# Performance work log

Hardware: AMD Instinct MI355X
Metric: run time of the kernel (lower is better)

## Reference

```python
import jax, jax.numpy as jnp
import numpy as np
from jax import lax

NUM_CLASSES = 2
NUM_PROTO = 10
C = 720


def _conv(x, w, b, pad):
    # x: [B,Cin,H,W], w: [Cout,Cin,kh,kw]
    y = lax.conv_general_dilated(x, w, (1, 1), ((pad, pad), (pad, pad)),
                                 dimension_numbers=('NCHW', 'OIHW', 'NCHW'))
    return y + b[None, :, None, None]


def _bn(x, g, b, rm, rv):
    inv = g / jnp.sqrt(rv + 1e-5)
    return (x - rm[None, :, None, None]) * inv[None, :, None, None] + b[None, :, None, None]


def _ln(x, g, b):
    mu = jnp.mean(x, -1, keepdims=True)
    var = jnp.var(x, -1, keepdims=True)
    return (x - mu) / jnp.sqrt(var + 1e-5) * g + b


def _l2n(x):
    n = jnp.linalg.norm(x, axis=-1, keepdims=True)
    return x / jnp.maximum(n, 1e-12)


def _resize_bilinear_ac(x, oh, ow):
    # bilinear with align_corners=True, x: [B,C,H,W]
    B, Cc, H, W = x.shape
    ys = jnp.linspace(0.0, H - 1.0, oh)
    xs = jnp.linspace(0.0, W - 1.0, ow)
    y0 = jnp.floor(ys).astype(jnp.int32)
    y1 = jnp.minimum(y0 + 1, H - 1)
    wy = (ys - y0).astype(x.dtype)
    x0 = jnp.floor(xs).astype(jnp.int32)
    x1 = jnp.minimum(x0 + 1, W - 1)
    wx = (xs - x0).astype(x.dtype)
    r = x[:, :, y0, :] * (1 - wy)[None, None, :, None] + x[:, :, y1, :] * wy[None, None, :, None]
    return r[:, :, :, x0] * (1 - wx) + r[:, :, :, x1] * wx


def setup_inputs() -> dict:
    key = jax.random.key(0)
    ks = jax.random.split(key, 8)
    B, H = 2, 96
    f32 = jnp.float32
    return {
        'feat1': jax.random.normal(ks[0], (B, 48, H, H), f32),
        'feat2': jax.random.normal(ks[1], (B, 96, H // 2, H // 2), f32),
        'feat3': jax.random.normal(ks[2], (B, 192, H // 4, H // 4), f32),
        'feat4': jax.random.normal(ks[3], (B, 384, H // 8, H // 8), f32),
        'cls_w': jax.random.normal(ks[4], (C, C, 3, 3), f32) * 0.02,
        'cls_b': jnp.zeros((C,), f32),
        'cls_bn_g': jnp.ones((C,), f32),
        'cls_bn_b': jnp.zeros((C,), f32),
        'cls_bn_rm': jnp.zeros((C,), f32),
        'cls_bn_rv': jnp.ones((C,), f32),
        'proj_w1': jax.random.normal(ks[5], (C, C, 1, 1), f32) * 0.02,
        'proj_b1': jnp.zeros((C,), f32),
        'proj_bn_g': jnp.ones((C,), f32),
        'proj_bn_b': jnp.zeros((C,), f32),
        'proj_bn_rm': jnp.zeros((C,), f32),
        'proj_bn_rv': jnp.ones((C,), f32),
        'proj_w2': jax.random.normal(ks[6], (C, C, 1, 1), f32) * 0.02,
        'proj_b2': jnp.zeros((C,), f32),
        'ln_feat_g': jnp.ones((C,), f32),
        'ln_feat_b': jnp.zeros((C,), f32),
        'ln_mask_g': jnp.ones((NUM_CLASSES,), f32),
        'ln_mask_b': jnp.zeros((NUM_CLASSES,), f32),
        'prototypes': jax.random.normal(ks[7], (NUM_CLASSES, NUM_PROTO, C), f32) * 0.02,
    }


def reference(feat1, feat2, feat3, feat4, cls_w, cls_b, cls_bn_g, cls_bn_b, cls_bn_rm,
              cls_bn_rv, proj_w1, proj_b1, proj_bn_g, proj_bn_b, proj_bn_rm, proj_bn_rv,
              proj_w2, proj_b2, ln_feat_g, ln_feat_b, ln_mask_g, ln_mask_b, prototypes):
    B, _, h, w = feat1.shape
    feats = jnp.concatenate([
        feat1,
        _resize_bilinear_ac(feat2, h, w),
        _resize_bilinear_ac(feat3, h, w),
        _resize_bilinear_ac(feat4, h, w),
    ], axis=1)  # [B,720,h,w]
    # cls_head: Conv3x3 + BN + ReLU (Dropout2d is identity in eval)
    c = jax.nn.relu(_bn(_conv(feats, cls_w, cls_b, 1), cls_bn_g, cls_bn_b, cls_bn_rm, cls_bn_rv))
    # proj_head (convmlp): Conv1x1 + BN + ReLU + Conv1x1
    p = jax.nn.relu(_bn(_conv(c, proj_w1, proj_b1, 0), proj_bn_g, proj_bn_b, proj_bn_rm, proj_bn_rv))
    p = _conv(p, proj_w2, proj_b2, 0)
    # (b h w) c
    _c = p.transpose(0, 2, 3, 1).reshape(-1, C)
    _c = _l2n(_ln(_c, ln_feat_g, ln_feat_b))
    protos = _l2n(prototypes)  # [K,M,C]
    masks = jnp.einsum('nd,kmd->nmk', _c, protos)  # [N,M,K]
    out_seg = jnp.max(masks, axis=1)               # [N,K]
    out_seg = _ln(out_seg, ln_mask_g, ln_mask_b)
    out_seg = out_seg.reshape(B, h, w, NUM_CLASSES).transpose(0, 3, 1, 2)
    return out_seg
```

## Files before the change

kernel.cpp:

```cpp
#include <hip/hip_runtime.h>
#include <float.h>

#define WDIM 96
#define HW   9216
#define PH   98
#define IMG  (PH*PH)
#define NPIXP (2*IMG)
#define NPIX 19328
#define GUARD 128
#define GPIX (NPIX + 2*GUARD)
#define NKG_ACT 96
#define MDIM 768
#define G3 816
#define G1 96

typedef _Float16 f16;
typedef f16  f16x8 __attribute__((ext_vector_type(8)));
typedef f16  f16x4 __attribute__((ext_vector_type(4)));
typedef float f32x4 __attribute__((ext_vector_type(4)));
typedef unsigned int u32;

typedef __attribute__((address_space(1))) const u32 gu32;
typedef __attribute__((address_space(3))) u32 lu32;
__device__ __forceinline__ void gld16(const f16* g, f16* s)
{
    __builtin_amdgcn_global_load_lds((gu32*)g, (lu32*)s, 16, 0, 0);
}

__global__ void prep_kernel(
    const float* __restrict__ cls_b,
    const float* __restrict__ g0, const float* __restrict__ b0,
    const float* __restrict__ rm0, const float* __restrict__ rv0,
    const float* __restrict__ p1b,
    const float* __restrict__ g1, const float* __restrict__ b1,
    const float* __restrict__ rm1, const float* __restrict__ rv1,
    const float* __restrict__ p2b,
    const float* __restrict__ protos,
    float* __restrict__ alpha, float* __restrict__ beta,
    float* __restrict__ protoN)
{
    __shared__ float red[4];
    if (blockIdx.x == 0) {
        for (int i = threadIdx.x; i < MDIM; i += blockDim.x) {
            if (i < 720) {
                float s0 = g0[i] * rsqrtf(rv0[i] + 1e-5f);
                alpha[i] = s0;
                beta[i]  = (cls_b[i] - rm0[i]) * s0 + b0[i];
                float s1 = g1[i] * rsqrtf(rv1[i] + 1e-5f);
                alpha[MDIM + i] = s1;
                beta[MDIM + i]  = (p1b[i] - rm1[i]) * s1 + b1[i];
                alpha[2*MDIM + i] = 1.0f;
                beta[2*MDIM + i]  = p2b[i];
            } else {
                alpha[i] = 0.f; beta[i] = 0.f;
                alpha[MDIM + i] = 0.f; beta[MDIM + i] = 0.f;
                alpha[2*MDIM + i] = 0.f; beta[2*MDIM + i] = 0.f;
            }
        }
    } else {
        int row = blockIdx.x - 1;
        const float* src = protos + row * 720;
        float s = 0.f;
        for (int i = threadIdx.x; i < 720; i += blockDim.x) { float v = src[i]; s += v * v; }
        #pragma unroll
        for (int off = 32; off > 0; off >>= 1) s += __shfl_down(s, off);
        int wave = threadIdx.x >> 6, lane = threadIdx.x & 63;
        if (lane == 0) red[wave] = s;
        __syncthreads();
        float tot = red[0] + red[1] + red[2] + red[3];
        float rn = 1.0f / fmaxf(sqrtf(tot), 1e-12f);
        for (int i = threadIdx.x; i < 720; i += blockDim.x)
            protoN[row * 720 + i] = src[i] * rn;
    }
}

__global__ __launch_bounds__(256)
void w3trans_kernel(const float* __restrict__ w3,
                    f16* __restrict__ W3h, f16* __restrict__ W3l)
{
    int tid = blockIdx.x * blockDim.x + threadIdx.x;
    int kgl = tid / MDIM;
    int o   = tid - kgl * MDIM;
    if (kgl > 90) return;

    if (kgl == 90) {
        f16x8 z = {0, 0, 0, 0, 0, 0, 0, 0};
        for (int g = 810; g < G3; ++g) {
            size_t off = ((size_t)g * MDIM + o) * 8;
            *(f16x8*)(W3h + off) = z;
            *(f16x8*)(W3l + off) = z;
        }
        return;
    }

    float buf[72];
    if (o < 720) {
        const float* src = w3 + (size_t)o * 6480 + kgl * 72;
        #pragma unroll
        for (int c = 0; c < 72; ++c) buf[c] = src[c];
    } else {
        #pragma unroll
        for (int c = 0; c < 72; ++c) buf[c] = 0.f;
    }

    #pragma unroll
    for (int s = 0; s < 9; ++s) {
        f16x8 hv, lv;
        #pragma unroll
        for (int c = 0; c < 8; ++c) {
            float v = buf[c * 9 + s];
            f16 h = (f16)v;
            hv[c] = h;
            lv[c] = (f16)(v - (float)h);
        }
        size_t off = ((size_t)(kgl * 9 + s) * MDIM + o) * 8;
        *(f16x8*)(W3h + off) = hv;
        *(f16x8*)(W3l + off) = lv;
    }
}

__global__ void w1trans_kernel(const float* __restrict__ w1a,
                               const float* __restrict__ w1b,
                               f16* __restrict__ W1ah, f16* __restrict__ W1al,
                               f16* __restrict__ W1bh, f16* __restrict__ W1bl)
{
    int tid = blockIdx.x * blockDim.x + threadIdx.x;
    const int N1 = G1 * MDIM;
    const float* src; f16 *dh, *dl; int g, o;
    if (tid < N1)            { g = tid / MDIM; o = tid - g * MDIM; src = w1a; dh = W1ah; dl = W1al; }
    else if (tid < 2 * N1)   { int u = tid - N1; g = u / MDIM; o = u - g * MDIM; src = w1b; dh = W1bh; dl = W1bl; }
    else return;

    float v[8];
    #pragma unroll
    for (int j = 0; j < 8; ++j) v[j] = 0.f;
    if (g < 90 && o < 720) {
        #pragma unroll
        for (int j = 0; j < 8; ++j)
            v[j] = src[(size_t)o * 720 + g * 8 + j];
    }
    f16x8 hv, lv;
    #pragma unroll
    for (int j = 0; j < 8; ++j) {
        f16 h = (f16)v[j];
        hv[j] = h;
        lv[j] = (f16)(v[j] - (float)h);
    }
    size_t off = ((size_t)g * MDIM + o) * 8;
    *(f16x8*)(dh + off) = hv;
    *(f16x8*)(dl + off) = lv;
}

__global__ void upsample_kernel(const float* __restrict__ f1,
                                const float* __restrict__ f2,
                                const float* __restrict__ f3,
                                const float* __restrict__ f4,
                                f16* __restrict__ Xhi, f16* __restrict__ Xlo)
{
    int tid = blockIdx.x * blockDim.x + threadIdx.x;
    if (tid >= 90 * GPIX) return;
    int kg = tid / GPIX;
    int gp = tid - kg * GPIX;
    int p  = gp - GUARD;
    float v[8];
    #pragma unroll
    for (int j = 0; j < 8; ++j) v[j] = 0.f;
    if (p >= 0 && p < NPIXP) {
        int b = p / IMG; int rem = p - b * IMG;
        int y = rem / PH; int x = rem - y * PH;
        if (y >= 1 && y <= 96 && x >= 1 && x <= 96) {
            int oy = y - 1, ox = x - 1;
            int c0 = kg * 8;
            if (c0 < 48) {
                #pragma unroll
                for (int j = 0; j < 8; ++j)
                    v[j] = f1[((size_t)(b * 48 + c0 + j)) * HW + oy * 96 + ox];
            } else {
                const float* src; int Cs, Hs, cb;
                if (c0 < 144)      { src = f2; Cs = 96;  Hs = 48; cb = c0 - 48; }
                else if (c0 < 336) { src = f3; Cs = 192; Hs = 24; cb = c0 - 144; }
                else               { src = f4; Cs = 384; Hs = 12; cb = c0 - 336; }
                float scale = (float)(Hs - 1) / 95.0f;
                float yf = oy * scale, xf = ox * scale;
                int y0 = (int)yf, x0 = (int)xf;
                float wy = yf - y0, wx = xf - x0;
                int y1 = min(y0 + 1, Hs - 1), x1 = min(x0 + 1, Hs - 1);
                #pragma unroll
                for (int j = 0; j < 8; ++j) {
                    const float* sb = src + (size_t)(b * Cs + cb + j) * Hs * Hs;
                    float v00 = sb[y0 * Hs + x0], v01 = sb[y0 * Hs + x1];
                    float v10 = sb[y1 * Hs + x0], v11 = sb[y1 * Hs + x1];
                    float r0 = v00 * (1.f - wy) + v10 * wy;
                    float r1 = v01 * (1.f - wy) + v11 * wy;
                    v[j] = r0 * (1.f - wx) + r1 * wx;
                }
            }
        }
    }
    f16x8 hv, lv;
    #pragma unroll
    for (int j = 0; j < 8; ++j) {
        f16 h = (f16)v[j];
        hv[j] = h;
        lv[j] = (f16)(v[j] - (float)h);
    }
    size_t off = (size_t)tid * 8;
    *(f16x8*)(Xhi + off) = hv;
    *(f16x8*)(Xlo + off) = lv;
}

template<int NSTEP, int CONV3>
__global__ __launch_bounds__(256, 2)
void mfma_gemm(const f16* __restrict__ Whi, const f16* __restrict__ Wlo,
               const f16* __restrict__ Bhi_, const f16* __restrict__ Blo_,
               f16* __restrict__ Ohi, f16* __restrict__ Olo,
               const float* __restrict__ alpha, const float* __restrict__ beta,
               int relu)
{
    __shared__ f16 sA[2][4][2][128][8];
    __shared__ f16 sB[2][4][2][128][8];

    const int l = blockIdx.x;
    const int xcd = l & 7;
    const int j0 = l >> 3;
    const int ncol = xcd * 19 + j0 / 6;
    if (ncol >= 151) return;
    const int m0 = (j0 % 6) * 128;
    const int n0 = ncol * 128;

    const int t = threadIdx.x;
    const int lane = t & 63, wid = t >> 6;
    const int wm = wid >> 1, wn = wid & 1;
    const int quad = lane >> 4, ln = lane & 15;

    f32x4 acc[4][4];
    #pragma unroll
    for (int i = 0; i < 4; ++i)
        #pragma unroll
        for (int j = 0; j < 4; ++j)
            acc[i][j] = (f32x4){0.f, 0.f, 0.f, 0.f};

    const f16* aH0 = Whi + ((size_t)wid * MDIM + m0 + lane) * 8;
    const f16* aL0 = Wlo + ((size_t)wid * MDIM + m0 + lane) * 8;
    const size_t aAdv = (size_t)4 * MDIM * 8;

    auto stage = [&](int st, int b) {
        const f16* ah = aH0 + (size_t)st * aAdv;
        const f16* al = aL0 + (size_t)st * aAdv;
        f16* dA = &sA[b][wid][0][0][0];
        gld16(ah,       dA);
        gld16(ah + 512, dA + 512);
        gld16(al,       dA + 1024);
        gld16(al + 512, dA + 1536);
        const int g = 4 * st + wid;
        long long brow;
        if (CONV3) {
            int gc = g > 809 ? 809 : g;
            int kgl = gc / 9;
            int s2 = gc - kgl * 9;
            brow = (long long)kgl * GPIX + (s2 / 3 - 1) * PH + (s2 % 3 - 1);
        } else {
            int gc = g > G1 - 1 ? G1 - 1 : g;
            brow = (long long)gc * GPIX;
        }
        const f16* bh = Bhi_ + (brow + n0 + lane) * 8;
        const f16* bl = Blo_ + (brow + n0 + lane) * 8;
        f16* dB = &sB[b][wid][0][0][0];
        gld16(bh,       dB);
        gld16(bh + 512, dB + 512);
        gld16(bl,       dB + 1024);
        gld16(bl + 512, dB + 1536);
    };

    stage(0, 0);
    __syncthreads();

    #pragma unroll 2
    for (int s = 0; s < NSTEP; ++s) {
        stage(s + 1, (s + 1) & 1);

        const int cur = s & 1;
        f16x8 av[8], bv[8];
        #pragma unroll
        for (int mt = 0; mt < 4; ++mt) {
            av[mt]     = *(const f16x8*)&sA[cur][quad][0][wm * 64 + mt * 16 + ln][0];
            av[mt + 4] = *(const f16x8*)&sA[cur][quad][1][wm * 64 + mt * 16 + ln][0];
            bv[mt]     = *(const f16x8*)&sB[cur][quad][0][wn * 64 + mt * 16 + ln][0];
            bv[mt + 4] = *(const f16x8*)&sB[cur][quad][1][wn * 64 + mt * 16 + ln][0];
        }
        #pragma unroll
        for (int mt = 0; mt < 4; ++mt)
            #pragma unroll
            for (int nt = 0; nt < 4; ++nt) {
                acc[mt][nt] = __builtin_amdgcn_mfma_f32_16x16x32_f16(av[mt],     bv[nt],     acc[mt][nt], 0, 0, 0);
                acc[mt][nt] = __builtin_amdgcn_mfma_f32_16x16x32_f16(av[mt],     bv[nt + 4], acc[mt][nt], 0, 0, 0);
                acc[mt][nt] = __builtin_amdgcn_mfma_f32_16x16x32_f16(av[mt + 4], bv[nt],     acc[mt][nt], 0, 0, 0);
            }

        __syncthreads();
    }

    #pragma unroll
    for (int mt = 0; mt < 4; ++mt) {
        const int rowb = m0 + wm * 64 + mt * 16 + quad * 4;
        const float4 a4 = *(const float4*)(alpha + rowb);
        const float4 b4 = *(const float4*)(beta + rowb);
        const size_t kg = rowb >> 3;
        const int sub = rowb & 7;
        #pragma unroll
        for (int nt = 0; nt < 4; ++nt) {
            const int P = n0 + wn * 64 + nt * 16 + ln;
            float v0 = acc[mt][nt][0] * a4.x + b4.x;
            float v1 = acc[mt][nt][1] * a4.y + b4.y;
            float v2 = acc[mt][nt][2] * a4.z + b4.z;
            float v3 = acc[mt][nt][3] * a4.w + b4.w;
            if (relu) {
                v0 = fmaxf(v0, 0.f); v1 = fmaxf(v1, 0.f);
                v2 = fmaxf(v2, 0.f); v3 = fmaxf(v3, 0.f);
            }
            f16 h0 = (f16)v0, h1 = (f16)v1, h2 = (f16)v2, h3 = (f16)v3;
            f16x4 hv = {h0, h1, h2, h3};
            f16x4 lv = {(f16)(v0 - (float)h0), (f16)(v1 - (float)h1),
                        (f16)(v2 - (float)h2), (f16)(v3 - (float)h3)};
            size_t o = (kg * GPIX + P) * 8 + sub;
            *(f16x4*)(Ohi + o) = hv;
            *(f16x4*)(Olo + o) = lv;
        }
    }
}

__global__ __launch_bounds__(256)
void head_kernel(const f16* __restrict__ Yhi, const f16* __restrict__ Ylo,
                 const float* __restrict__ lng, const float* __restrict__ lnb,
                 const float* __restrict__ protoN,
                 const float* __restrict__ lmg, const float* __restrict__ lmb,
                 float* __restrict__ out)
{
    const int t = threadIdx.x;
    const int wv = t >> 6, lane = t & 63;
    const int pw = lane >> 4, sub = lane & 15;
    const int p = blockIdx.x * 16 + wv * 4 + pw;
    const int b = p / HW; const int r = p - b * HW;
    const int y = r / 96; const int x = r - y * 96;
    const size_t P = (size_t)b * IMG + (y + 1) * PH + (x + 1);

    f16x8 xh[6], xl[6];
    float s1 = 0.f, s2 = 0.f;
    #pragma unroll
    for (int k = 0; k < 6; ++k) {
        int kg = sub + 16 * k;
        if (kg < 90) {
            xh[k] = *(const f16x8*)(Yhi + ((size_t)kg * GPIX + P) * 8);
            xl[k] = *(const f16x8*)(Ylo + ((size_t)kg * GPIX + P) * 8);
            #pragma unroll
            for (int j = 0; j < 8; ++j) {
                float v = (float)xh[k][j] + (float)xl[k][j];
                s1 += v; s2 += v * v;
            }
        }
    }
    #pragma unroll
    for (int m = 1; m < 16; m <<= 1) {
        s1 += __shfl_xor(s1, m);
        s2 += __shfl_xor(s2, m);
    }
    float mu  = s1 * (1.0f / 720.0f);
    float var = s2 * (1.0f / 720.0f) - mu * mu;
    float inv = rsqrtf(var + 1e-5f);

    float dots[20];
    #pragma unroll
    for (int q = 0; q < 20; ++q) dots[q] = 0.f;
    float nrm = 0.f;
    #pragma unroll
    for (int k = 0; k < 6; ++k) {
        int kg = sub + 16 * k;
        if (kg < 90) {
            const int c0 = kg * 8;
            #pragma unroll
            for (int j = 0; j < 8; ++j) {
                const int c = c0 + j;
                float v = ((float)xh[k][j] + (float)xl[k][j] - mu) * inv * lng[c] + lnb[c];
                nrm += v * v;
                #pragma unroll
                for (int q = 0; q < 20; ++q)
                    dots[q] = fmaf(v, protoN[q * 720 + c], dots[q]);
            }
        }
    }
    #pragma unroll
    for (int m = 1; m < 16; m <<= 1) {
        nrm += __shfl_xor(nrm, m);
        #pragma unroll
        for (int q = 0; q < 20; ++q) dots[q] += __shfl_xor(dots[q], m);
    }

    if (sub == 0) {
        float rn = 1.0f / fmaxf(sqrtf(nrm), 1e-12f);
        float m0v = -FLT_MAX, m1v = -FLT_MAX;
        #pragma unroll
        for (int q = 0; q < 10; ++q) m0v = fmaxf(m0v, dots[q]);
        #pragma unroll
        for (int q = 10; q < 20; ++q) m1v = fmaxf(m1v, dots[q]);
        m0v *= rn; m1v *= rn;
        float mu2 = 0.5f * (m0v + m1v);
        float dv  = m0v - mu2;
        float va  = dv * dv;
        float iv  = rsqrtf(va + 1e-5f);
        float o0 = (m0v - mu2) * iv * lmg[0] + lmb[0];
        float o1 = (m1v - mu2) * iv * lmg[1] + lmb[1];
        out[b * (2 * HW) + r]      = o0;
        out[b * (2 * HW) + HW + r] = o1;
    }
}

extern "C" void kernel_launch(void* const* d_in, const int* in_sizes, int n_in,
                              void* d_out, int out_size, void* d_ws, size_t ws_size,
                              hipStream_t stream)
{
    const float* feat1      = (const float*)d_in[0];
    const float* feat2      = (const float*)d_in[1];
    const float* feat3      = (const float*)d_in[2];
    const float* feat4      = (const float*)d_in[3];
    const float* cls_w      = (const float*)d_in[4];
    const float* cls_b      = (const float*)d_in[5];
    const float* cls_bn_g   = (const float*)d_in[6];
    const float* cls_bn_b   = (const float*)d_in[7];
    const float* cls_bn_rm  = (const float*)d_in[8];
    const float* cls_bn_rv  = (const float*)d_in[9];
    const float* proj_w1    = (const float*)d_in[10];
    const float* proj_b1    = (const float*)d_in[11];
    const float* proj_bn_g  = (const float*)d_in[12];
    const float* proj_bn_b  = (const float*)d_in[13];
    const float* proj_bn_rm = (const float*)d_in[14];
    const float* proj_bn_rv = (const float*)d_in[15];
    const float* proj_w2    = (const float*)d_in[16];
    const float* proj_b2    = (const float*)d_in[17];
    const float* ln_feat_g  = (const float*)d_in[18];
    const float* ln_feat_b  = (const float*)d_in[19];
    const float* ln_mask_g  = (const float*)d_in[20];
    const float* ln_mask_b  = (const float*)d_in[21];
    const float* protos     = (const float*)d_in[22];

    const size_t PLANEH = (size_t)NKG_ACT * GPIX * 8;
    const size_t W3SZ   = (size_t)G3 * MDIM * 8;
    const size_t W1SZ   = (size_t)G1 * MDIM * 8;

    f16* Xhi  = (f16*)d_ws;
    f16* Xlo  = Xhi + PLANEH;
    f16* Yhi  = Xlo + PLANEH;
    f16* Ylo  = Yhi + PLANEH;
    f16* W3h  = Ylo + PLANEH;
    f16* W3l  = W3h + W3SZ;
    f16* W1ah = W3l + W3SZ;
    f16* W1al = W1ah + W1SZ;
    f16* W1bh = W1al + W1SZ;
    f16* W1bl = W1bh + W1SZ;
    float* alphas = (float*)(W1bl + W1SZ);
    float* betas  = alphas + 3 * MDIM;
    float* protoN = betas + 3 * MDIM;

    prep_kernel<<<21, 256, 0, stream>>>(cls_b, cls_bn_g, cls_bn_b, cls_bn_rm, cls_bn_rv,
                                        proj_b1, proj_bn_g, proj_bn_b, proj_bn_rm, proj_bn_rv,
                                        proj_b2, protos, alphas, betas, protoN);
    {
        int total = 91 * MDIM;
        w3trans_kernel<<<(total + 255) / 256, 256, 0, stream>>>(cls_w, W3h, W3l);
    }
    {
        int total = 2 * G1 * MDIM;
        w1trans_kernel<<<(total + 255) / 256, 256, 0, stream>>>(proj_w1, proj_w2,
                                                                W1ah, W1al, W1bh, W1bl);
    }
    {
        int total = 90 * GPIX;
        upsample_kernel<<<(total + 255) / 256, 256, 0, stream>>>(feat1, feat2, feat3, feat4,
                                                                 Xhi, Xlo);
    }

    const size_t GOFF = (size_t)GUARD * 8;
    const int NBLK = 912;
    mfma_gemm<203, 1><<<NBLK, 256, 0, stream>>>(W3h, W3l, Xhi + GOFF, Xlo + GOFF,
                                                Yhi + GOFF, Ylo + GOFF,
                                                alphas, betas, 1);
    mfma_gemm<23, 0><<<NBLK, 256, 0, stream>>>(W1ah, W1al, Yhi + GOFF, Ylo + GOFF,
                                               Xhi + GOFF, Xlo + GOFF,
                                               alphas + MDIM, betas + MDIM, 1);
    mfma_gemm<23, 0><<<NBLK, 256, 0, stream>>>(W1bh, W1bl, Xhi + GOFF, Xlo + GOFF,
                                               Yhi + GOFF, Ylo + GOFF,
                                               alphas + 2 * MDIM, betas + 2 * MDIM, 0);

    head_kernel<<<HW * 2 / 16, 256, 0, stream>>>(Yhi + GOFF, Ylo + GOFF,
                                                 ln_feat_g, ln_feat_b, protoN,
                                                 ln_mask_g, ln_mask_b, (float*)d_out);
}
```

Baseline: 771.0 us.

## Switch GEMM to 32x32x16 MFMA with single-buffered LDS and higher occupancy

Replaces the 16x16x32 MFMA tiling with 32x32x16 MFMA instructions, so each wave holds a 2x2 grid of 32x32 accumulators. The LDS double buffer becomes a single buffer: fragments are read into registers, a barrier is taken, and then the next stage is issued before the MFMAs run. Launch bounds are raised to 4 blocks per CU. The aim is fewer LDS reads per FLOP and more resident waves to hide latency. In exchange it adds a second barrier per step, and each stage's load now has less time to complete before the next iteration reads it.

```diff
diff --git a/kernel.cpp b/kernel.cpp
--- a/kernel.cpp
+++ b/kernel.cpp
@@ -18,6 +18,7 @@
 typedef f16  f16x8 __attribute__((ext_vector_type(8)));
 typedef f16  f16x4 __attribute__((ext_vector_type(4)));
 typedef float f32x4 __attribute__((ext_vector_type(4)));
+typedef float f32x16 __attribute__((ext_vector_type(16)));
 typedef unsigned int u32;
 
 typedef __attribute__((address_space(1))) const u32 gu32;
@@ -210,15 +211,15 @@
 }
 
 template<int NSTEP, int CONV3>
-__global__ __launch_bounds__(256, 2)
+__global__ __launch_bounds__(256, 4)
 void mfma_gemm(const f16* __restrict__ Whi, const f16* __restrict__ Wlo,
                const f16* __restrict__ Bhi_, const f16* __restrict__ Blo_,
                f16* __restrict__ Ohi, f16* __restrict__ Olo,
                const float* __restrict__ alpha, const float* __restrict__ beta,
                int relu)
 {
-    __shared__ f16 sA[2][4][2][128][8];
-    __shared__ f16 sB[2][4][2][128][8];
+    __shared__ f16 sA[4][2][128][8];
+    __shared__ f16 sB[4][2][128][8];
 
     const int l = blockIdx.x;
     const int xcd = l & 7;
@@ -231,23 +232,24 @@
     const int t = threadIdx.x;
     const int lane = t & 63, wid = t >> 6;
     const int wm = wid >> 1, wn = wid & 1;
-    const int quad = lane >> 4, ln = lane & 15;
-
-    f32x4 acc[4][4];
-    #pragma unroll
-    for (int i = 0; i < 4; ++i)
-        #pragma unroll
-        for (int j = 0; j < 4; ++j)
-            acc[i][j] = (f32x4){0.f, 0.f, 0.f, 0.f};
+    const int l31 = lane & 31, lk = lane >> 5;
+
+    f32x16 acc[2][2];
+    #pragma unroll
+    for (int i = 0; i < 2; ++i)
+        #pragma unroll
+        for (int j = 0; j < 2; ++j)
+            acc[i][j] = (f32x16){0.f,0.f,0.f,0.f,0.f,0.f,0.f,0.f,
+                                 0.f,0.f,0.f,0.f,0.f,0.f,0.f,0.f};
 
     const f16* aH0 = Whi + ((size_t)wid * MDIM + m0 + lane) * 8;
     const f16* aL0 = Wlo + ((size_t)wid * MDIM + m0 + lane) * 8;
     const size_t aAdv = (size_t)4 * MDIM * 8;
 
-    auto stage = [&](int st, int b) {
+    auto stage = [&](int st) {
         const f16* ah = aH0 + (size_t)st * aAdv;
         const f16* al = aL0 + (size_t)st * aAdv;
-        f16* dA = &sA[b][wid][0][0][0];
+        f16* dA = &sA[wid][0][0][0];
         gld16(ah,       dA);
         gld16(ah + 512, dA + 512);
         gld16(al,       dA + 1024);
@@ -265,68 +267,76 @@
         }
         const f16* bh = Bhi_ + (brow + n0 + lane) * 8;
         const f16* bl = Blo_ + (brow + n0 + lane) * 8;
-        f16* dB = &sB[b][wid][0][0][0];
+        f16* dB = &sB[wid][0][0][0];
         gld16(bh,       dB);
         gld16(bh + 512, dB + 512);
         gld16(bl,       dB + 1024);
         gld16(bl + 512, dB + 1536);
     };
 
-    stage(0, 0);
+    stage(0);
     __syncthreads();
 
-    #pragma unroll 2
+    #pragma unroll 1
     for (int s = 0; s < NSTEP; ++s) {
-        stage(s + 1, (s + 1) & 1);
-
-        const int cur = s & 1;
-        f16x8 av[8], bv[8];
-        #pragma unroll
-        for (int mt = 0; mt < 4; ++mt) {
-            av[mt]     = *(const f16x8*)&sA[cur][quad][0][wm * 64 + mt * 16 + ln][0];
-            av[mt + 4] = *(const f16x8*)&sA[cur][quad][1][wm * 64 + mt * 16 + ln][0];
-            bv[mt]     = *(const f16x8*)&sB[cur][quad][0][wn * 64 + mt * 16 + ln][0];
-            bv[mt + 4] = *(const f16x8*)&sB[cur][quad][1][wn * 64 + mt * 16 + ln][0];
-        }
-        #pragma unroll
-        for (int mt = 0; mt < 4; ++mt)
+        f16x8 avh[2][2], avl[2][2], bvh[2][2], bvl[2][2];
+        #pragma unroll
+        for (int gp = 0; gp < 2; ++gp)
             #pragma unroll
-            for (int nt = 0; nt < 4; ++nt) {
-                acc[mt][nt] = __builtin_amdgcn_mfma_f32_16x16x32_f16(av[mt],     bv[nt],     acc[mt][nt], 0, 0, 0);
-                acc[mt][nt] = __builtin_amdgcn_mfma_f32_16x16x32_f16(av[mt],     bv[nt + 4], acc[mt][nt], 0, 0, 0);
-                acc[mt][nt] = __builtin_amdgcn_mfma_f32_16x16x32_f16(av[mt + 4], bv[nt],     acc[mt][nt], 0, 0, 0);
+            for (int mt = 0; mt < 2; ++mt) {
+                avh[gp][mt] = *(const f16x8*)&sA[2*gp + lk][0][wm*64 + mt*32 + l31][0];
+                avl[gp][mt] = *(const f16x8*)&sA[2*gp + lk][1][wm*64 + mt*32 + l31][0];
+                bvh[gp][mt] = *(const f16x8*)&sB[2*gp + lk][0][wn*64 + mt*32 + l31][0];
+                bvl[gp][mt] = *(const f16x8*)&sB[2*gp + lk][1][wn*64 + mt*32 + l31][0];
             }
 
         __syncthreads();
-    }
-
-    #pragma unroll
-    for (int mt = 0; mt < 4; ++mt) {
-        const int rowb = m0 + wm * 64 + mt * 16 + quad * 4;
-        const float4 a4 = *(const float4*)(alpha + rowb);
-        const float4 b4 = *(const float4*)(beta + rowb);
-        const size_t kg = rowb >> 3;
-        const int sub = rowb & 7;
-        #pragma unroll
-        for (int nt = 0; nt < 4; ++nt) {
-            const int P = n0 + wn * 64 + nt * 16 + ln;
-            float v0 = acc[mt][nt][0] * a4.x + b4.x;
-            float v1 = acc[mt][nt][1] * a4.y + b4.y;
-            float v2 = acc[mt][nt][2] * a4.z + b4.z;
-            float v3 = acc[mt][nt][3] * a4.w + b4.w;
-            if (relu) {
-                v0 = fmaxf(v0, 0.f); v1 = fmaxf(v1, 0.f);
-                v2 = fmaxf(v2, 0.f); v3 = fmaxf(v3, 0.f);
+
+        stage(s + 1);
+
+        #pragma unroll
+        for (int gp = 0; gp < 2; ++gp)
+            #pragma unroll
+            for (int mt = 0; mt < 2; ++mt)
+                #pragma unroll
+                for (int nt = 0; nt < 2; ++nt) {
+                    acc[mt][nt] = __builtin_amdgcn_mfma_f32_32x32x16_f16(avh[gp][mt], bvh[gp][nt], acc[mt][nt], 0, 0, 0);
+                    acc[mt][nt] = __builtin_amdgcn_mfma_f32_32x32x16_f16(avh[gp][mt], bvl[gp][nt], acc[mt][nt], 0, 0, 0);
+                    acc[mt][nt] = __builtin_amdgcn_mfma_f32_32x32x16_f16(avl[gp][mt], bvh[gp][nt], acc[mt][nt], 0, 0, 0);
+                }
+
+        __syncthreads();
+    }
+
+    #pragma unroll
+    for (int mt = 0; mt < 2; ++mt)
+        #pragma unroll
+        for (int nt = 0; nt < 2; ++nt) {
+            const int P = n0 + wn * 64 + nt * 32 + l31;
+            #pragma unroll
+            for (int q = 0; q < 4; ++q) {
+                const int rowb = m0 + wm * 64 + mt * 32 + q * 8 + lk * 4;
+                const float4 a4 = *(const float4*)(alpha + rowb);
+                const float4 b4 = *(const float4*)(beta + rowb);
+                const size_t kg = rowb >> 3;
+                const int sub = rowb & 7;
+                float v0 = acc[mt][nt][q*4 + 0] * a4.x + b4.x;
+                float v1 = acc[mt][nt][q*4 + 1] * a4.y + b4.y;
+                float v2 = acc[mt][nt][q*4 + 2] * a4.z + b4.z;
+                float v3 = acc[mt][nt][q*4 + 3] * a4.w + b4.w;
+                if (relu) {
+                    v0 = fmaxf(v0, 0.f); v1 = fmaxf(v1, 0.f);
+                    v2 = fmaxf(v2, 0.f); v3 = fmaxf(v3, 0.f);
+                }
+                f16 h0 = (f16)v0, h1 = (f16)v1, h2 = (f16)v2, h3 = (f16)v3;
+                f16x4 hv = {h0, h1, h2, h3};
+                f16x4 lv = {(f16)(v0 - (float)h0), (f16)(v1 - (float)h1),
+                            (f16)(v2 - (float)h2), (f16)(v3 - (float)h3)};
+                size_t o = (kg * GPIX + P) * 8 + sub;
+                *(f16x4*)(Ohi + o) = hv;
+                *(f16x4*)(Olo + o) = lv;
             }
-            f16 h0 = (f16)v0, h1 = (f16)v1, h2 = (f16)v2, h3 = (f16)v3;
-            f16x4 hv = {h0, h1, h2, h3};
-            f16x4 lv = {(f16)(v0 - (float)h0), (f16)(v1 - (float)h1),
-                        (f16)(v2 - (float)h2), (f16)(v3 - (float)h3)};
-            size_t o = (kg * GPIX + P) * 8 + sub;
-            *(f16x4*)(Ohi + o) = hv;
-            *(f16x4*)(Olo + o) = lv;
-        }
-    }
+        }
 }
 
 __global__ __launch_bounds__(256)
```

After: 859.7 us. 1.12x slower.

## Software-pipeline GEMM mainloop with register double-buffered fragments and prefetch depth two

Applied to the files above, without the earlier changes.

Restructures the GEMM main loop so global-to-LDS loads run two stages ahead, and the LDS fragment reads for the next step overlap with the MFMAs of the current step. Fragments are double-buffered in registers. Explicit vmcnt/lgkmcnt waits, raw s_barrier, sched_barrier and setprio are used in place of __syncthreads. The padded K-group counts grow so the extra prefetch stays in bounds, and the 1x1 clamp is hardcoded to 89. This costs more VGPRs and depends on the hand-tuned waitcnt values being correct.

```diff
diff --git a/kernel.cpp b/kernel.cpp
--- a/kernel.cpp
+++ b/kernel.cpp
@@ -11,8 +11,8 @@
 #define GPIX (NPIX + 2*GUARD)
 #define NKG_ACT 96
 #define MDIM 768
-#define G3 816
-#define G1 96
+#define G3 824
+#define G1 104
 
 typedef _Float16 f16;
 typedef f16  f16x8 __attribute__((ext_vector_type(8)));
@@ -244,10 +244,10 @@
     const f16* aL0 = Wlo + ((size_t)wid * MDIM + m0 + lane) * 8;
     const size_t aAdv = (size_t)4 * MDIM * 8;
 
-    auto stage = [&](int st, int b) {
+    auto stage = [&](int st, int slot) {
         const f16* ah = aH0 + (size_t)st * aAdv;
         const f16* al = aL0 + (size_t)st * aAdv;
-        f16* dA = &sA[b][wid][0][0][0];
+        f16* dA = &sA[slot][wid][0][0][0];
         gld16(ah,       dA);
         gld16(ah + 512, dA + 512);
         gld16(al,       dA + 1024);
@@ -260,34 +260,29 @@
             int s2 = gc - kgl * 9;
             brow = (long long)kgl * GPIX + (s2 / 3 - 1) * PH + (s2 % 3 - 1);
         } else {
-            int gc = g > G1 - 1 ? G1 - 1 : g;
+            int gc = g > 89 ? 89 : g;
             brow = (long long)gc * GPIX;
         }
         const f16* bh = Bhi_ + (brow + n0 + lane) * 8;
         const f16* bl = Blo_ + (brow + n0 + lane) * 8;
-        f16* dB = &sB[b][wid][0][0][0];
+        f16* dB = &sB[slot][wid][0][0][0];
         gld16(bh,       dB);
         gld16(bh + 512, dB + 512);
         gld16(bl,       dB + 1024);
         gld16(bl + 512, dB + 1536);
     };
 
-    stage(0, 0);
-    __syncthreads();
-
-    #pragma unroll 2
-    for (int s = 0; s < NSTEP; ++s) {
-        stage(s + 1, (s + 1) & 1);
-
-        const int cur = s & 1;
-        f16x8 av[8], bv[8];
+    auto read_frags = [&](f16x8 (&a)[8], f16x8 (&b)[8], int c) {
         #pragma unroll
         for (int mt = 0; mt < 4; ++mt) {
-            av[mt]     = *(const f16x8*)&sA[cur][quad][0][wm * 64 + mt * 16 + ln][0];
-            av[mt + 4] = *(const f16x8*)&sA[cur][quad][1][wm * 64 + mt * 16 + ln][0];
-            bv[mt]     = *(const f16x8*)&sB[cur][quad][0][wn * 64 + mt * 16 + ln][0];
-            bv[mt + 4] = *(const f16x8*)&sB[cur][quad][1][wn * 64 + mt * 16 + ln][0];
-        }
+            a[mt]     = *(const f16x8*)&sA[c][quad][0][wm * 64 + mt * 16 + ln][0];
+            a[mt + 4] = *(const f16x8*)&sA[c][quad][1][wm * 64 + mt * 16 + ln][0];
+            b[mt]     = *(const f16x8*)&sB[c][quad][0][wn * 64 + mt * 16 + ln][0];
+            b[mt + 4] = *(const f16x8*)&sB[c][quad][1][wn * 64 + mt * 16 + ln][0];
+        }
+    };
+
+    auto compute = [&](f16x8 (&av)[8], f16x8 (&bv)[8]) {
         #pragma unroll
         for (int mt = 0; mt < 4; ++mt)
             #pragma unroll
@@ -296,9 +291,42 @@
                 acc[mt][nt] = __builtin_amdgcn_mfma_f32_16x16x32_f16(av[mt],     bv[nt + 4], acc[mt][nt], 0, 0, 0);
                 acc[mt][nt] = __builtin_amdgcn_mfma_f32_16x16x32_f16(av[mt + 4], bv[nt],     acc[mt][nt], 0, 0, 0);
             }
-
-        __syncthreads();
-    }
+    };
+
+    f16x8 aP[8], bP[8], aQ[8], bQ[8];
+
+    auto body = [&](int s, f16x8 (&pa)[8], f16x8 (&pb)[8],
+                           f16x8 (&qa)[8], f16x8 (&qb)[8]) {
+        stage(s + 2, s & 1);
+        asm volatile("s_waitcnt vmcnt(8)" ::: "memory");
+        __builtin_amdgcn_s_barrier();
+        read_frags(qa, qb, (s + 1) & 1);
+        __builtin_amdgcn_sched_barrier(0);
+        __builtin_amdgcn_s_setprio(1);
+        compute(pa, pb);
+        __builtin_amdgcn_s_setprio(0);
+        asm volatile("s_waitcnt lgkmcnt(0)" ::: "memory");
+        __builtin_amdgcn_sched_barrier(0);
+        __builtin_amdgcn_s_barrier();
+    };
+
+    stage(0, 0);
+    stage(1, 1);
+    asm volatile("s_waitcnt vmcnt(8)" ::: "memory");
+    __builtin_amdgcn_s_barrier();
+    read_frags(aP, bP, 0);
+    asm volatile("s_waitcnt lgkmcnt(0)" ::: "memory");
+    __builtin_amdgcn_sched_barrier(0);
+    __builtin_amdgcn_s_barrier();
+
+    int s = 0;
+    #pragma unroll 1
+    for (; s + 1 < NSTEP; s += 2) {
+        body(s,     aP, bP, aQ, bQ);
+        body(s + 1, aQ, bQ, aP, bP);
+    }
+    if (s < NSTEP)
+        body(s, aP, bP, aQ, bQ);
 
     #pragma unroll
     for (int mt = 0; mt < 4; ++mt) {
```

Result: faster. 734.3 us (-4.8%).
